# Performance work log

Hardware: AMD Instinct MI355X
Metric: run time of the kernel (lower is better)

Reference implementation:

```python
import jax, jax.numpy as jnp
import numpy as np

B = 512; D = 128; NL = 16; LAYERS = 4; H = 4; HD = D // H
MAX_D = 128; MAX_E = 512
N_DRUG = 25600; N_ENZ = 153600


def setup_inputs() -> dict:
    key = jax.random.key(0)
    ks = jax.random.split(key, 40)
    it = iter(range(40))
    def nrm(shape, scale=0.02):
        return jax.random.normal(ks[next(it)], shape, jnp.float32) * scale
    inp = {}
    inp["drug_k"] = jax.random.normal(ks[next(it)], (N_DRUG, D), jnp.float32)
    inp["drug_v"] = jax.random.normal(ks[next(it)], (N_DRUG, D), jnp.float32)
    inp["enzyme_k"] = jax.random.normal(ks[next(it)], (N_ENZ, D), jnp.float32)
    inp["enzyme_v"] = jax.random.normal(ks[next(it)], (N_ENZ, D), jnp.float32)
    inp["drug_batch"] = jnp.sort(jax.random.randint(ks[next(it)], (N_DRUG,), 0, B))
    inp["enzyme_batch"] = jnp.sort(jax.random.randint(ks[next(it)], (N_ENZ,), 0, B))
    inp["latents"] = nrm((1, NL, D), 1.0)
    inp["wq_d"] = nrm((LAYERS, D, D)); inp["bq_d"] = jnp.zeros((LAYERS, D), jnp.float32)
    inp["wq_e"] = nrm((LAYERS, D, D)); inp["bq_e"] = jnp.zeros((LAYERS, D), jnp.float32)
    inp["mha_d_w"] = nrm((LAYERS, 3 * D, D)); inp["mha_d_b"] = jnp.zeros((LAYERS, 3 * D), jnp.float32)
    inp["mha_d_ow"] = nrm((LAYERS, D, D)); inp["mha_d_ob"] = jnp.zeros((LAYERS, D), jnp.float32)
    inp["mha_e_w"] = nrm((LAYERS, 3 * D, D)); inp["mha_e_b"] = jnp.zeros((LAYERS, 3 * D), jnp.float32)
    inp["mha_e_ow"] = nrm((LAYERS, D, D)); inp["mha_e_ob"] = jnp.zeros((LAYERS, D), jnp.float32)
    inp["ln1_g"] = jnp.ones((LAYERS, D), jnp.float32); inp["ln1_b"] = jnp.zeros((LAYERS, D), jnp.float32)
    inp["ln2_g"] = jnp.ones((LAYERS, D), jnp.float32); inp["ln2_b"] = jnp.zeros((LAYERS, D), jnp.float32)
    inp["ffn_w1"] = nrm((LAYERS, 2 * D, D)); inp["ffn_b1"] = jnp.zeros((LAYERS, 2 * D), jnp.float32)
    inp["ffn_w2"] = nrm((LAYERS, D, 2 * D)); inp["ffn_b2"] = jnp.zeros((LAYERS, D), jnp.float32)
    inp["head_w1"] = nrm((D, D * NL)); inp["head_b1"] = jnp.zeros((D,), jnp.float32)
    inp["head_w2"] = nrm((1, D)); inp["head_b2"] = jnp.zeros((1,), jnp.float32)
    return inp


def to_dense(x, batch, max_len):
    # PyG to_dense_batch: ragged [N, D] -> padded [B, max_len, D] + bool mask
    ones = jnp.ones_like(batch)
    counts = jax.ops.segment_sum(ones, batch, num_segments=B)
    starts = jnp.concatenate([jnp.zeros((1,), counts.dtype), jnp.cumsum(counts)[:-1]])
    pos = jnp.arange(batch.shape[0]) - starts[batch]
    dense = jnp.zeros((B, max_len, x.shape[-1]), x.dtype).at[batch, pos].set(x)
    mask = jnp.zeros((B, max_len), bool).at[batch, pos].set(True)
    return dense, mask


def layer_norm(x, g, b):
    m = x.mean(-1, keepdims=True)
    v = ((x - m) ** 2).mean(-1, keepdims=True)
    return (x - m) / jnp.sqrt(v + 1e-5) * g + b


def mha(q, k, v, mask, w, b, ow, ob):
    # torch nn.MultiheadAttention (batch_first) with key_padding_mask (~mask = ignore)
    wq, wk, wv = w[:D], w[D:2 * D], w[2 * D:]
    bq, bk, bv = b[:D], b[D:2 * D], b[2 * D:]
    qh = (q @ wq.T + bq).reshape(q.shape[0], -1, H, HD)
    kh = (k @ wk.T + bk).reshape(k.shape[0], -1, H, HD)
    vh = (v @ wv.T + bv).reshape(v.shape[0], -1, H, HD)
    s = jnp.einsum('bqhd,bkhd->bhqk', qh, kh) / jnp.sqrt(jnp.float32(HD))
    s = jnp.where(mask[:, None, None, :], s, jnp.float32(-1e9))
    a = jax.nn.softmax(s, axis=-1)
    o = jnp.einsum('bhqk,bkhd->bqhd', a, vh).reshape(q.shape[0], -1, D)
    return o @ ow.T + ob


def forward_impl(drug_k, drug_v, enzyme_k, enzyme_v, latents,
                 wq_d, bq_d, wq_e, bq_e,
                 mha_d_w, mha_d_b, mha_d_ow, mha_d_ob,
                 mha_e_w, mha_e_b, mha_e_ow, mha_e_ob,
                 ln1_g, ln1_b, ln2_g, ln2_b,
                 ffn_w1, ffn_b1, ffn_w2, ffn_b2,
                 head_w1, head_b1, head_w2, head_b2,
                 drug_batch, enzyme_batch):
    dK, dM = to_dense(drug_k, drug_batch, MAX_D)
    dV, _ = to_dense(drug_v, drug_batch, MAX_D)
    eK, eM = to_dense(enzyme_k, enzyme_batch, MAX_E)
    eV, _ = to_dense(enzyme_v, enzyme_batch, MAX_E)
    lat = jnp.broadcast_to(latents, (B, NL, D))
    for l in range(LAYERS):
        nl = layer_norm(lat, ln1_g[l], ln1_b[l])
        q_d = nl @ wq_d[l].T + bq_d[l]
        q_e = nl @ wq_e[l].T + bq_e[l]
        ad = mha(q_d, dK, dV, dM, mha_d_w[l], mha_d_b[l], mha_d_ow[l], mha_d_ob[l])
        ae = mha(q_e, eK, eV, eM, mha_e_w[l], mha_e_b[l], mha_e_ow[l], mha_e_ob[l])
        lat = lat + ad + ae
        h = layer_norm(lat, ln2_g[l], ln2_b[l])
        h = jax.nn.relu(h @ ffn_w1[l].T + ffn_b1[l]) @ ffn_w2[l].T + ffn_b2[l]
        lat = lat + h
    flat = lat.reshape(B, NL * D)
    h = jax.nn.relu(flat @ head_w1.T + head_b1)
    return jax.nn.softplus(h @ head_w2.T + head_b2)[:, 0]


def reference(drug_k, drug_v, enzyme_k, enzyme_v, drug_batch, enzyme_batch, latents,
              wq_d, bq_d, wq_e, bq_e,
              mha_d_w, mha_d_b, mha_d_ow, mha_d_ob,
              mha_e_w, mha_e_b, mha_e_ow, mha_e_ob,
              ln1_g, ln1_b, ln2_g, ln2_b,
              ffn_w1, ffn_b1, ffn_w2, ffn_b2,
              head_w1, head_b1, head_w2, head_b2):
    return forward_impl(drug_k, drug_v, enzyme_k, enzyme_v, latents,
                        wq_d, bq_d, wq_e, bq_e,
                        mha_d_w, mha_d_b, mha_d_ow, mha_d_ob,
                        mha_e_w, mha_e_b, mha_e_ow, mha_e_ob,
                        ln1_g, ln1_b, ln2_g, ln2_b,
                        ffn_w1, ffn_b1, ffn_w2, ffn_b2,
                        head_w1, head_b1, head_w2, head_b2,
                        drug_batch, enzyme_batch)
```

## Files before the change

kernel.cpp:

```cpp
#include <hip/hip_runtime.h>
#include <math.h>

#define NL 16
#define DD 128

typedef __attribute__((ext_vector_type(8))) short short8;
typedef __attribute__((ext_vector_type(4))) float floatx4;

union U8 { short8 v; unsigned short s[8]; };

__device__ __forceinline__ unsigned short f2bf(float x) {
  union { float f; unsigned u; } v; v.f = x; return (unsigned short)(v.u >> 16);
}
__device__ __forceinline__ float bf2f(unsigned short s) {
  union { unsigned u; float f; } v; v.u = ((unsigned)s) << 16; return v.f;
}

__global__ void seg_kernel(const int* __restrict__ db, int nd,
                           const int* __restrict__ eb, int ne,
                           int* __restrict__ seg) {
  const int* arr = (blockIdx.x == 0) ? db : eb;
  int n = (blockIdx.x == 0) ? nd : ne;
  int* start = seg + blockIdx.x * 1024;
  int* cnt = start + 512;
  int b = threadIdx.x;
  if (b < 512) {
    int lo = 0, hi = n;
    while (lo < hi) { int mid = (lo + hi) >> 1; if (arr[mid] < b) lo = mid + 1; else hi = mid; }
    int s = lo;
    lo = s; hi = n;
    while (lo < hi) { int mid = (lo + hi) >> 1; if (arr[mid] < b + 1) lo = mid + 1; else hi = mid; }
    start[b] = s; cnt[b] = lo - s;
  }
}

__global__ void init_lat_kernel(const float* __restrict__ latents, float* __restrict__ lat) {
  int i = blockIdx.x * blockDim.x + threadIdx.x;
  ((float4*)lat)[i] = ((const float4*)latents)[i & 511];
}

__global__ void cvt4_kernel(const float* __restrict__ a, unsigned short* __restrict__ da, int na4,
                            const float* __restrict__ b, unsigned short* __restrict__ db, int nb4,
                            const float* __restrict__ c, unsigned short* __restrict__ dc, int nc4,
                            const float* __restrict__ d, unsigned short* __restrict__ dd, int nd4) {
  int i = blockIdx.x * blockDim.x + threadIdx.x;
  const float* s; unsigned short* o; int r;
  if (i < na4)                        { s = a; o = da; r = i; }
  else if (i < na4 + nb4)             { s = b; o = db; r = i - na4; }
  else if (i < na4 + nb4 + nc4)       { s = c; o = dc; r = i - na4 - nb4; }
  else if (i < na4 + nb4 + nc4 + nd4) { s = d; o = dd; r = i - na4 - nb4 - nc4; }
  else return;
  float4 v = ((const float4*)s)[r];
  ushort4 u = { f2bf(v.x), f2bf(v.y), f2bf(v.z), f2bf(v.w) };
  ((ushort4*)o)[r] = u;
}

__global__ void cvtw_kernel(const float* __restrict__ mw_d, const float* __restrict__ ow_d,
                            const float* __restrict__ mw_e, const float* __restrict__ ow_e,
                            const float* __restrict__ w1, const float* __restrict__ w2,
                            unsigned short* __restrict__ Wbf) {
  int l = blockIdx.x >> 7, blk = blockIdx.x & 127;
  int idx = blk * 1024 + threadIdx.x * 4;
  const float* src; int off;
  if (idx < 16384)      { src = mw_d + (size_t)l * 49152 + 32768; off = idx; }
  else if (idx < 32768) { src = ow_d + (size_t)l * 16384; off = idx - 16384; }
  else if (idx < 49152) { src = mw_e + (size_t)l * 49152 + 32768; off = idx - 32768; }
  else if (idx < 65536) { src = ow_e + (size_t)l * 16384; off = idx - 49152; }
  else if (idx < 98304) { src = w1 + (size_t)l * 32768; off = idx - 65536; }
  else                  { src = w2 + (size_t)l * 32768; off = idx - 98304; }
  float4 v = *(const float4*)(src + off);
  ushort4 o = { f2bf(v.x), f2bf(v.y), f2bf(v.z), f2bf(v.w) };
  *(ushort4*)(Wbf + (size_t)l * 131072 + idx) = o;
}

__global__ __launch_bounds__(256) void fold_kernel(
    const float* __restrict__ wq_d, const float* __restrict__ bq_d,
    const float* __restrict__ wq_e, const float* __restrict__ bq_e,
    const float* __restrict__ mw_d, const float* __restrict__ mb_d,
    const float* __restrict__ mw_e, const float* __restrict__ mb_e,
    float* __restrict__ Wqf, float* __restrict__ bqf) {
  __shared__ __align__(16) float sMW[2048];
  const int pb = blockIdx.x >> 3, rg = blockIdx.x & 7;
  const int l = pb >> 1, p = pb & 1;
  const float* wq = (p == 0 ? wq_d : wq_e) + (size_t)l * 16384;
  const float* bq = (p == 0 ? bq_d : bq_e) + l * 128;
  const float* mw = (p == 0 ? mw_d : mw_e) + (size_t)l * 49152;
  const float* mb = (p == 0 ? mb_d : mb_e) + l * 384;
  const float scale = 0.17677669529663687f;
  const int tid = threadIdx.x;
  {
    const float4* src = (const float4*)(mw + rg * 2048);
    ((float4*)sMW)[tid] = src[tid];
    ((float4*)sMW)[tid + 256] = src[tid + 256];
  }
  __syncthreads();
  const int j = tid & 127, ih = tid >> 7;
  float acc[8];
#pragma unroll
  for (int r = 0; r < 8; ++r) acc[r] = 0.f;
#pragma unroll 4
  for (int k = 0; k < 128; ++k) {
    float wv = wq[k * 128 + j];
#pragma unroll
    for (int r = 0; r < 8; ++r) acc[r] += sMW[(ih * 8 + r) * 128 + k] * wv;
  }
  float* W = Wqf + (size_t)pb * 16384 + (rg * 16 + ih * 8) * 128 + j;
#pragma unroll
  for (int r = 0; r < 8; ++r) W[r * 128] = acc[r] * scale;
  if (rg == 0 && tid < 128) {
    float s = 0.f;
    const float* mr = mw + tid * 128;
    for (int k = 0; k < 128; ++k) s += mr[k] * bq[k];
    bqf[pb * 128 + tid] = (s + mb[tid]) * scale;
  }
}

__global__ __launch_bounds__(256) void wt_kernel(
    const float* __restrict__ Wqf, const float* __restrict__ bqf,
    const float* __restrict__ mw_d, const float* __restrict__ mw_e,
    unsigned short* __restrict__ WtB, float* __restrict__ bt) {
  const int l = blockIdx.x >> 3, p = (blockIdx.x >> 2) & 1, h = blockIdx.x & 3;
  const float* wqf = Wqf + (size_t)(l * 2 + p) * 16384 + (h * 32) * 128;
  const float* wk  = (p == 0 ? mw_d : mw_e) + (size_t)l * 49152 + 16384 + (h * 32) * 128;
  const float* bqv = bqf + (l * 2 + p) * 128 + h * 32;
  __shared__ __align__(16) float sWq[4096];
  __shared__ __align__(16) float sWk[4096];
  __shared__ float sBq[32];
  const int tid = threadIdx.x;
  for (int i = tid; i < 1024; i += 256) {
    ((float4*)sWq)[i] = ((const float4*)wqf)[i];
    ((float4*)sWk)[i] = ((const float4*)wk)[i];
  }
  if (tid < 32) sBq[tid] = bqv[tid];
  __syncthreads();
  const int d = tid & 127, kh = tid >> 7;
  const int n = p * 512 + h * 128 + d;
  const int tn = n >> 4, m = n & 15;
  unsigned short* outl = WtB + (size_t)l * 131072;
#pragma unroll
  for (int kc = 0; kc < 4; ++kc) {
    int k0 = kh * 64 + kc * 16;
    float acc[16];
#pragma unroll
    for (int kk = 0; kk < 16; ++kk) acc[kk] = 0.f;
    for (int j = 0; j < 32; ++j) {
      float wkd = sWk[j * 128 + d];
#pragma unroll
      for (int kk = 0; kk < 16; ++kk) acc[kk] += sWq[j * 128 + k0 + kk] * wkd;
    }
#pragma unroll
    for (int kk = 0; kk < 16; ++kk) {
      int k = k0 + kk;
      int c = k >> 5, quad = (k >> 3) & 3, j8 = k & 7;
      int lane = quad * 16 + m;
      outl[(((size_t)tn * 4 + c) * 64 + lane) * 8 + j8] = f2bf(acc[kk]);
    }
  }
  if (kh == 0) {
    float a = 0.f;
    for (int j = 0; j < 32; ++j) a += sBq[j] * sWk[j * 128 + d];
    bt[l * 1024 + n] = a;
  }
}

__global__ __launch_bounds__(256) void qtilde_kernel(
    const float* __restrict__ lat,
    const float* __restrict__ lng, const float* __restrict__ lnb,
    const unsigned short* __restrict__ WtBl, const float* __restrict__ btl,
    unsigned short* __restrict__ Qt) {
  __shared__ __align__(16) unsigned short sNL[16 * 136];
  const int tid = threadIdx.x;
  const int b = blockIdx.x;
  {
    int q = tid >> 4, li = tid & 15, d0 = li * 8;
    const float* xr = lat + ((size_t)b * NL + q) * DD + d0;
    float x[8];
    *(float4*)(x) = *(const float4*)(xr);
    *(float4*)(x + 4) = *(const float4*)(xr + 4);
    float s1 = 0.f, s2 = 0.f;
#pragma unroll
    for (int j = 0; j < 8; ++j) { s1 += x[j]; s2 += x[j] * x[j]; }
#pragma unroll
    for (int o = 1; o < 16; o <<= 1) { s1 += __shfl_xor(s1, o); s2 += __shfl_xor(s2, o); }
    float mean = s1 * (1.f / 128.f);
    float var = s2 * (1.f / 128.f) - mean * mean;
    float rstd = rsqrtf(var + 1e-5f);
    float y[8];
#pragma unroll
    for (int j = 0; j < 8; ++j)
      y[j] = (x[j] - mean) * rstd * lng[d0 + j] + lnb[d0 + j];
    ushort4 o0 = { f2bf(y[0]), f2bf(y[1]), f2bf(y[2]), f2bf(y[3]) };
    ushort4 o1 = { f2bf(y[4]), f2bf(y[5]), f2bf(y[6]), f2bf(y[7]) };
    *(ushort4*)(sNL + q * 136 + d0) = o0;
    *(ushort4*)(sNL + q * 136 + d0 + 4) = o1;
  }
  __syncthreads();
  const int lane = tid & 63, w = tid >> 6, m = lane & 15, quad = lane >> 4;
  short8 aF[4];
  {
    const unsigned short* arow = sNL + m * 136 + quad * 8;
#pragma unroll
    for (int c = 0; c < 4; ++c) aF[c] = *(const short8*)(arow + c * 32);
  }
  unsigned short* qtb = Qt + (size_t)b * 16384;
#pragma unroll
  for (int t = 0; t < 16; ++t) {
    int tn = w * 16 + t;
    floatx4 acc = (floatx4){0.f, 0.f, 0.f, 0.f};
#pragma unroll
    for (int c = 0; c < 4; ++c) {
      short8 bF = *(const short8*)(WtBl + (((size_t)tn * 4 + c) * 64 + lane) * 8);
      acc = __builtin_amdgcn_mfma_f32_16x16x32_bf16(aF[c], bF, acc, 0, 0, 0);
    }
    int n = tn * 16 + m;
    float bb = btl[n];
    int p = n >> 9, h = (n >> 7) & 3, d = n & 127;
    unsigned short* op = qtb + (p * 64 + h * 16) * 128 + d;
#pragma unroll
    for (int r = 0; r < 4; ++r) op[(quad * 4 + r) * 128] = f2bf(acc[r] + bb);
  }
}

__global__ __launch_bounds__(256, 4) void attn3_kernel(
    const unsigned short* __restrict__ Kd, const unsigned short* __restrict__ Vd,
    const unsigned short* __restrict__ Ke, const unsigned short* __restrict__ Ve,
    const int* __restrict__ seg,
    const unsigned short* __restrict__ Qt,
    unsigned short* __restrict__ part_d, float* __restrict__ l_d,
    unsigned short* __restrict__ part_e, float* __restrict__ l_e) {
  __shared__ __align__(16) unsigned short sK[32 * 136];
  __shared__ __align__(16) unsigned short sV[128 * 40];
  __shared__ __align__(16) unsigned short sP[64 * 40];
  const int tid = threadIdx.x;
  const int bi = blockIdx.x;

  const unsigned short* Kp; const unsigned short* Vp;
  const unsigned short* qt;
  unsigned short* part; float* lpart;
  int len, st;
  if (bi < 2048) {
    int b = bi >> 2, sp = bi & 3;
    int n = seg[1536 + b]; if (n > 512) n = 512;
    int chunk = (n + 3) >> 2;
    int begin = sp * chunk;
    len = n - begin; if (len > chunk) len = chunk; if (len < 0) len = 0;
    st = seg[1024 + b] + begin;
    Kp = Ke; Vp = Ve;
    qt = Qt + ((size_t)b * 2 + 1) * 8192;
    part = part_e + (size_t)bi * 8192;
    lpart = l_e + (size_t)bi * 64;
  } else {
    int b = bi - 2048;
    int n = seg[512 + b]; if (n > 128) n = 128;
    len = n;
    st = seg[b];
    Kp = Kd; Vp = Vd;
    qt = Qt + (size_t)b * 2 * 8192;
    part = part_d + (size_t)b * 8192;
    lpart = l_d + (size_t)b * 64;
  }

  const int lane = tid & 63;
  const int w = tid >> 6;
  const int m = lane & 15;
  const int quad = lane >> 4;

  short8 qA[4];
  {
    const unsigned short* qrow = qt + (size_t)(w * 16 + m) * 128 + quad * 8;
#pragma unroll
    for (int c = 0; c < 4; ++c) qA[c] = *(const short8*)(qrow + c * 32);
  }

  floatx4 oA[8];
#pragma unroll
  for (int i = 0; i < 8; ++i) oA[i] = (floatx4){0.f, 0.f, 0.f, 0.f};
  float lp[4] = {0.f, 0.f, 0.f, 0.f};

  short8 rK[2], rV[2];
  const short8 z8 = {0, 0, 0, 0, 0, 0, 0, 0};
  auto load_tile = [&](int t0) {
    int nv = len - t0; if (nv > 32) nv = 32;
#pragma unroll
    for (int it = 0; it < 2; ++it) {
      int f = tid + it * 256;
      int tok = f >> 4, d8 = f & 15;
      rK[it] = (tok < nv) ? *(const short8*)(Kp + (size_t)(st + t0 + tok) * 128 + d8 * 8) : z8;
    }
#pragma unroll
    for (int it = 0; it < 2; ++it) {
      int f = tid + it * 256;
      int tok = f & 31, d8 = f >> 5;
      rV[it] = (tok < nv) ? *(const short8*)(Vp + (size_t)(st + t0 + tok) * 128 + d8 * 8) : z8;
    }
  };
  auto store_tile = [&]() {
#pragma unroll
    for (int it = 0; it < 2; ++it) {
      int f = tid + it * 256;
      int tok = f >> 4, d8 = f & 15;
      *(short8*)(sK + tok * 136 + d8 * 8) = rK[it];
    }
#pragma unroll
    for (int it = 0; it < 2; ++it) {
      int f = tid + it * 256;
      int tok = f & 31, d8 = f >> 5;
      U8 u; u.v = rV[it];
#pragma unroll
      for (int j = 0; j < 8; ++j) sV[(d8 * 8 + j) * 40 + tok] = u.s[j];
    }
  };

  if (len > 0) load_tile(0);
  for (int t0 = 0; t0 < len; t0 += 32) {
    __syncthreads();
    store_tile();
    __syncthreads();
    if (t0 + 32 < len) load_tile(t0 + 32);
    int nv = len - t0; if (nv > 32) nv = 32;
    floatx4 sS[2];
    sS[0] = (floatx4){0.f, 0.f, 0.f, 0.f};
    sS[1] = (floatx4){0.f, 0.f, 0.f, 0.f};
#pragma unroll
    for (int g = 0; g < 2; ++g)
#pragma unroll
      for (int c = 0; c < 4; ++c) {
        short8 kB = *(const short8*)(sK + (g * 16 + m) * 136 + c * 32 + quad * 8);
        sS[g] = __builtin_amdgcn_mfma_f32_16x16x32_bf16(qA[c], kB, sS[g], 0, 0, 0);
      }
#pragma unroll
    for (int g = 0; g < 2; ++g) {
      bool valid = (g * 16 + m) < nv;
#pragma unroll
      for (int r = 0; r < 4; ++r) {
        float p = valid ? __expf(sS[g][r]) : 0.f;
        lp[r] += p;
        sP[(w * 16 + quad * 4 + r) * 40 + g * 16 + m] = f2bf(p);
      }
    }
    short8 pA = *(const short8*)(sP + (w * 16 + m) * 40 + quad * 8);
#pragma unroll
    for (int dg = 0; dg < 8; ++dg) {
      short8 vB = *(const short8*)(sV + (dg * 16 + m) * 40 + quad * 8);
      oA[dg] = __builtin_amdgcn_mfma_f32_16x16x32_bf16(pA, vB, oA[dg], 0, 0, 0);
    }
  }

#pragma unroll
  for (int r = 0; r < 4; ++r) {
    float v = lp[r];
    v += __shfl_xor(v, 1); v += __shfl_xor(v, 2);
    v += __shfl_xor(v, 4); v += __shfl_xor(v, 8);
    lp[r] = v;
  }
  if (m == 0) {
#pragma unroll
    for (int r = 0; r < 4; ++r)
      lpart[w * 16 + quad * 4 + r] = lp[r];
  }
#pragma unroll
  for (int dg = 0; dg < 8; ++dg)
#pragma unroll
    for (int r = 0; r < 4; ++r)
      part[(w * 16 + quad * 4 + r) * 128 + dg * 16 + m] = f2bf(oA[dg][r]);
}

__global__ __launch_bounds__(256) void post_kernel(
    const unsigned short* __restrict__ pd, const float* __restrict__ ldv,
    const unsigned short* __restrict__ pe, const float* __restrict__ lev,
    const unsigned short* __restrict__ Wl,
    const float* __restrict__ bv_d, const float* __restrict__ ob_d,
    const float* __restrict__ bv_e, const float* __restrict__ ob_e,
    const float* __restrict__ ln2g, const float* __restrict__ ln2b,
    const float* __restrict__ b1, const float* __restrict__ b2,
    float* __restrict__ lat) {
  const unsigned short* wv_d = Wl;
  const unsigned short* ow_d = Wl + 16384;
  const unsigned short* wv_e = Wl + 32768;
  const unsigned short* ow_e = Wl + 49152;
  const unsigned short* w1   = Wl + 65536;
  const unsigned short* w2   = Wl + 98304;

  __shared__ __align__(16) unsigned short sX[64 * 136];
  __shared__ __align__(16) unsigned short sVH[16 * 136];
  __shared__ __align__(16) unsigned short sF[16 * 264];
  __shared__ __align__(16) float sAcc[16 * 132];
  __shared__ float sLd[64], sLe[64];

  const int tid = threadIdx.x;
  const int b = blockIdx.x;
  const int lane = tid & 63;
  const int w = tid >> 6;
  const int m = lane & 15;
  const int quad = lane >> 4;

  if (tid < 64) {
    float v = ldv[(size_t)b * 64 + tid];
    sLd[tid] = (v > 0.f) ? 1.f / v : 0.f;
  } else if (tid < 128) {
    int r = tid - 64;
    float v = lev[((size_t)b * 4 + 0) * 64 + r] + lev[((size_t)b * 4 + 1) * 64 + r]
            + lev[((size_t)b * 4 + 2) * 64 + r] + lev[((size_t)b * 4 + 3) * 64 + r];
    sLe[r] = (v > 0.f) ? 1.f / v : 0.f;
  }
  __syncthreads();
  {
    const ushort4* src = (const ushort4*)(pd + (size_t)b * 8192);
#pragma unroll
    for (int it = 0; it < 8; ++it) {
      int f = tid + it * 256;
      int row = f >> 5, d = (f & 31) * 4;
      ushort4 u = src[f];
      float sc = sLd[row];
      ushort4 o = { f2bf(bf2f(u.x) * sc), f2bf(bf2f(u.y) * sc),
                    f2bf(bf2f(u.z) * sc), f2bf(bf2f(u.w) * sc) };
      *(ushort4*)(sX + row * 136 + d) = o;
    }
  }
  __syncthreads();
  {
    short8 aF[4];
    const unsigned short* arow = sX + (w * 16 + m) * 136 + quad * 8;
#pragma unroll
    for (int c = 0; c < 4; ++c) aF[c] = *(const short8*)(arow + c * 32);
#pragma unroll
    for (int t = 0; t < 2; ++t) {
      int n = w * 32 + t * 16 + m;
      floatx4 acc = (floatx4){0.f, 0.f, 0.f, 0.f};
      const unsigned short* brow = wv_d + n * 128 + quad * 8;
#pragma unroll
      for (int c = 0; c < 4; ++c)
        acc = __builtin_amdgcn_mfma_f32_16x16x32_bf16(aF[c], *(const short8*)(brow + c * 32), acc, 0, 0, 0);
      float bb = bv_d[n];
#pragma unroll
      for (int r = 0; r < 4; ++r) sVH[(quad * 4 + r) * 136 + n] = f2bf(acc[r] + bb);
    }
  }
  __syncthreads();
  {
    short8 aF[4];
    const unsigned short* arow = sVH + m * 136 + quad * 8;
#pragma unroll
    for (int c = 0; c < 4; ++c) aF[c] = *(const short8*)(arow + c * 32);
#pragma unroll
    for (int t = 0; t < 2; ++t) {
      int n = w * 32 + t * 16 + m;
      floatx4 acc = (floatx4){0.f, 0.f, 0.f, 0.f};
      const unsigned short* brow = ow_d + n * 128 + quad * 8;
#pragma unroll
      for (int c = 0; c < 4; ++c)
        acc = __builtin_amdgcn_mfma_f32_16x16x32_bf16(aF[c], *(const short8*)(brow + c * 32), acc, 0, 0, 0);
      float bb = ob_d[n];
#pragma unroll
      for (int r = 0; r < 4; ++r) {
        int q = quad * 4 + r;
        sAcc[q * 132 + n] = lat[(size_t)b * 2048 + q * 128 + n] + acc[r] + bb;
      }
    }
  }
  __syncthreads();
  {
    const ushort4* s0 = (const ushort4*)(pe + ((size_t)b * 4 + 0) * 8192);
    const ushort4* s1 = (const ushort4*)(pe + ((size_t)b * 4 + 1) * 8192);
    const ushort4* s2 = (const ushort4*)(pe + ((size_t)b * 4 + 2) * 8192);
    const ushort4* s3 = (const ushort4*)(pe + ((size_t)b * 4 + 3) * 8192);
#pragma unroll
    for (int it = 0; it < 8; ++it) {
      int f = tid + it * 256;
      int row = f >> 5, d = (f & 31) * 4;
      ushort4 u0 = s0[f], u1 = s1[f], u2 = s2[f], u3 = s3[f];
      float sc = sLe[row];
      ushort4 o = { f2bf((bf2f(u0.x) + bf2f(u1.x) + bf2f(u2.x) + bf2f(u3.x)) * sc),
                    f2bf((bf2f(u0.y) + bf2f(u1.y) + bf2f(u2.y) + bf2f(u3.y)) * sc),
                    f2bf((bf2f(u0.z) + bf2f(u1.z) + bf2f(u2.z) + bf2f(u3.z)) * sc),
                    f2bf((bf2f(u0.w) + bf2f(u1.w) + bf2f(u2.w) + bf2f(u3.w)) * sc) };
      *(ushort4*)(sX + row * 136 + d) = o;
    }
  }
  __syncthreads();
  {
    short8 aF[4];
    const unsigned short* arow = sX + (w * 16 + m) * 136 + quad * 8;
#pragma unroll
    for (int c = 0; c < 4; ++c) aF[c] = *(const short8*)(arow + c * 32);
#pragma unroll
    for (int t = 0; t < 2; ++t) {
      int n = w * 32 + t * 16 + m;
      floatx4 acc = (floatx4){0.f, 0.f, 0.f, 0.f};
      const unsigned short* brow = wv_e + n * 128 + quad * 8;
#pragma unroll
      for (int c = 0; c < 4; ++c)
        acc = __builtin_amdgcn_mfma_f32_16x16x32_bf16(aF[c], *(const short8*)(brow + c * 32), acc, 0, 0, 0);
      float bb = bv_e[n];
#pragma unroll
      for (int r = 0; r < 4; ++r) sVH[(quad * 4 + r) * 136 + n] = f2bf(acc[r] + bb);
    }
  }
  __syncthreads();
  {
    short8 aF[4];
    const unsigned short* arow = sVH + m * 136 + quad * 8;
#pragma unroll
    for (int c = 0; c < 4; ++c) aF[c] = *(const short8*)(arow + c * 32);
#pragma unroll
    for (int t = 0; t < 2; ++t) {
      int n = w * 32 + t * 16 + m;
      floatx4 acc = (floatx4){0.f, 0.f, 0.f, 0.f};
      const unsigned short* brow = ow_e + n * 128 + quad * 8;
#pragma unroll
      for (int c = 0; c < 4; ++c)
        acc = __builtin_amdgcn_mfma_f32_16x16x32_bf16(aF[c], *(const short8*)(brow + c * 32), acc, 0, 0, 0);
      float bb = ob_e[n];
#pragma unroll
      for (int r = 0; r < 4; ++r) {
        int q = quad * 4 + r;
        sAcc[q * 132 + n] += acc[r] + bb;
      }
    }
  }
  __syncthreads();
  {
    int q = tid >> 4, li = tid & 15, d0 = li * 8;
    float x[8];
#pragma unroll
    for (int j = 0; j < 8; ++j) x[j] = sAcc[q * 132 + d0 + j];
    float s1 = 0.f, s2 = 0.f;
#pragma unroll
    for (int j = 0; j < 8; ++j) { s1 += x[j]; s2 += x[j] * x[j]; }
#pragma unroll
    for (int o = 1; o < 16; o <<= 1) { s1 += __shfl_xor(s1, o); s2 += __shfl_xor(s2, o); }
    float mean = s1 * (1.f / 128.f);
    float var = s2 * (1.f / 128.f) - mean * mean;
    float rstd = rsqrtf(var + 1e-5f);
    float y[8];
#pragma unroll
    for (int j = 0; j < 8; ++j)
      y[j] = (x[j] - mean) * rstd * ln2g[d0 + j] + ln2b[d0 + j];
    ushort4 o0 = { f2bf(y[0]), f2bf(y[1]), f2bf(y[2]), f2bf(y[3]) };
    ushort4 o1 = { f2bf(y[4]), f2bf(y[5]), f2bf(y[6]), f2bf(y[7]) };
    *(ushort4*)(sX + q * 136 + d0) = o0;
    *(ushort4*)(sX + q * 136 + d0 + 4) = o1;
  }
  __syncthreads();
  {
    short8 aF[4];
    const unsigned short* arow = sX + m * 136 + quad * 8;
#pragma unroll
    for (int c = 0; c < 4; ++c) aF[c] = *(const short8*)(arow + c * 32);
#pragma unroll
    for (int t = 0; t < 4; ++t) {
      int n = w * 64 + t * 16 + m;
      floatx4 acc = (floatx4){0.f, 0.f, 0.f, 0.f};
      const unsigned short* brow = w1 + n * 128 + quad * 8;
#pragma unroll
      for (int c = 0; c < 4; ++c)
        acc = __builtin_amdgcn_mfma_f32_16x16x32_bf16(aF[c], *(const short8*)(brow + c * 32), acc, 0, 0, 0);
      float bb = b1[n];
#pragma unroll
      for (int r = 0; r < 4; ++r)
        sF[(quad * 4 + r) * 264 + n] = f2bf(fmaxf(acc[r] + bb, 0.f));
    }
  }
  __syncthreads();
  {
    short8 aF[8];
    const unsigned short* arow = sF + m * 264 + quad * 8;
#pragma unroll
    for (int c = 0; c < 8; ++c) aF[c] = *(const short8*)(arow + c * 32);
#pragma unroll
    for (int t = 0; t < 2; ++t) {
      int n = w * 32 + t * 16 + m;
      floatx4 acc = (floatx4){0.f, 0.f, 0.f, 0.f};
      const unsigned short* brow = w2 + n * 256 + quad * 8;
#pragma unroll
      for (int c = 0; c < 8; ++c)
        acc = __builtin_amdgcn_mfma_f32_16x16x32_bf16(aF[c], *(const short8*)(brow + c * 32), acc, 0, 0, 0);
      float bb = b2[n];
#pragma unroll
      for (int r = 0; r < 4; ++r) {
        int q = quad * 4 + r;
        lat[(size_t)b * 2048 + q * 128 + n] = sAcc[q * 132 + n] + acc[r] + bb;
      }
    }
  }
}

__global__ __launch_bounds__(256) void head_kernel(const float* __restrict__ lat,
                                                   const float* __restrict__ w1,
                                                   const float* __restrict__ b1,
                                                   const float* __restrict__ w2,
                                                   const float* __restrict__ b2,
                                                   float* __restrict__ out) {
  __shared__ __align__(16) float sX[2048];
  __shared__ float sH[128];
  const int tid = threadIdx.x;
  const int b = blockIdx.x;
  {
    const float4* src = (const float4*)(lat + (size_t)b * 2048);
#pragma unroll
    for (int it = 0; it < 2; ++it) ((float4*)sX)[tid + it * 256] = src[tid + it * 256];
  }
  __syncthreads();
  {
    int o = tid >> 1, kh = tid & 1;
    float a = 0.f;
    const float* wr = w1 + (size_t)o * 2048 + kh * 1024;
    const float* xb = sX + kh * 1024;
    for (int k4 = 0; k4 < 256; ++k4) {
      float4 w4 = *(const float4*)(wr + k4 * 4);
      float4 x4 = *(const float4*)(xb + k4 * 4);
      a += w4.x * x4.x + w4.y * x4.y + w4.z * x4.z + w4.w * x4.w;
    }
    a += __shfl_xor(a, 1);
    if (kh == 0) sH[o] = fmaxf(a + b1[o], 0.f);
  }
  __syncthreads();
  if (tid < 64) {
    float a = sH[tid] * w2[tid] + sH[tid + 64] * w2[tid + 64];
#pragma unroll
    for (int o = 1; o < 64; o <<= 1) a += __shfl_xor(a, o);
    if (tid == 0) {
      float x = a + b2[0];
      out[b] = (x > 20.f) ? x : log1pf(__expf(x));
    }
  }
}

extern "C" void kernel_launch(void* const* d_in, const int* in_sizes, int n_in,
                              void* d_out, int out_size, void* d_ws, size_t ws_size,
                              hipStream_t stream) {
  const float* drug_k  = (const float*)d_in[0];
  const float* drug_v  = (const float*)d_in[1];
  const float* enz_k   = (const float*)d_in[2];
  const float* enz_v   = (const float*)d_in[3];
  const int*   drug_b  = (const int*)d_in[4];
  const int*   enz_b   = (const int*)d_in[5];
  const float* latents = (const float*)d_in[6];
  const float* wq_d    = (const float*)d_in[7];
  const float* bq_d    = (const float*)d_in[8];
  const float* wq_e    = (const float*)d_in[9];
  const float* bq_e    = (const float*)d_in[10];
  const float* mha_d_w = (const float*)d_in[11];
  const float* mha_d_b = (const float*)d_in[12];
  const float* mha_d_ow= (const float*)d_in[13];
  const float* mha_d_ob= (const float*)d_in[14];
  const float* mha_e_w = (const float*)d_in[15];
  const float* mha_e_b = (const float*)d_in[16];
  const float* mha_e_ow= (const float*)d_in[17];
  const float* mha_e_ob= (const float*)d_in[18];
  const float* ln1_g   = (const float*)d_in[19];
  const float* ln1_b   = (const float*)d_in[20];
  const float* ln2_g   = (const float*)d_in[21];
  const float* ln2_b   = (const float*)d_in[22];
  const float* ffn_w1  = (const float*)d_in[23];
  const float* ffn_b1  = (const float*)d_in[24];
  const float* ffn_w2  = (const float*)d_in[25];
  const float* ffn_b2  = (const float*)d_in[26];
  const float* head_w1 = (const float*)d_in[27];
  const float* head_b1 = (const float*)d_in[28];
  const float* head_w2 = (const float*)d_in[29];
  const float* head_b2 = (const float*)d_in[30];
  float* out = (float*)d_out;

  const int n_dk = in_sizes[0];
  const int n_ek = in_sizes[2];

  int* seg = (int*)d_ws;
  float* fws = (float*)d_ws;
  float* Wqf = fws + 2048;
  float* bqf = Wqf + 131072;
  float* lat = bqf + 1024;
  float* l_d = lat + 1048576;
  float* l_e = l_d + 32768;
  unsigned short* Qt     = (unsigned short*)(l_e + 131072);
  unsigned short* part_d = Qt + 8388608;
  unsigned short* part_e = part_d + 4194304;
  unsigned short* Kd_bf  = part_e + 16777216;
  unsigned short* Vd_bf  = Kd_bf + n_dk;
  unsigned short* Ke_bf  = Vd_bf + n_dk;
  unsigned short* Ve_bf  = Ke_bf + n_ek;
  unsigned short* Wbf    = Ve_bf + n_ek;
  unsigned short* WtB    = Wbf + 524288;
  float* bt              = (float*)(WtB + 524288);

  seg_kernel<<<2, 512, 0, stream>>>(drug_b, in_sizes[4], enz_b, in_sizes[5], seg);
  init_lat_kernel<<<1024, 256, 0, stream>>>(latents, lat);
  fold_kernel<<<64, 256, 0, stream>>>(wq_d, bq_d, wq_e, bq_e,
                                      mha_d_w, mha_d_b, mha_e_w, mha_e_b, Wqf, bqf);
  wt_kernel<<<32, 256, 0, stream>>>(Wqf, bqf, mha_d_w, mha_e_w, WtB, bt);
  {
    int na4 = n_dk / 4, nc4 = n_ek / 4;
    int tot = na4 * 2 + nc4 * 2;
    cvt4_kernel<<<(tot + 255) / 256, 256, 0, stream>>>(
        drug_k, Kd_bf, na4, drug_v, Vd_bf, na4, enz_k, Ke_bf, nc4, enz_v, Ve_bf, nc4);
  }
  cvtw_kernel<<<512, 256, 0, stream>>>(mha_d_w, mha_d_ow, mha_e_w, mha_e_ow,
                                       ffn_w1, ffn_w2, Wbf);
  for (int l = 0; l < 4; ++l) {
    qtilde_kernel<<<512, 256, 0, stream>>>(lat, ln1_g + l * 128, ln1_b + l * 128,
        WtB + (size_t)l * 131072, bt + l * 1024, Qt);
    attn3_kernel<<<2560, 256, 0, stream>>>(Kd_bf, Vd_bf, Ke_bf, Ve_bf, seg,
        Qt, part_d, l_d, part_e, l_e);
    post_kernel<<<512, 256, 0, stream>>>(part_d, l_d, part_e, l_e,
        Wbf + (size_t)l * 131072,
        mha_d_b + l * 384 + 256, mha_d_ob + l * 128,
        mha_e_b + l * 384 + 256, mha_e_ob + l * 128,
        ln2_g + l * 128, ln2_b + l * 128,
        ffn_b1 + l * 256, ffn_b2 + l * 128,
        lat);
  }
  head_kernel<<<512, 256, 0, stream>>>(lat, head_w1, head_b1, head_w2, head_b2, out);
}
```

Measured before the change: 623.2 us.

## Fuse K/V bf16 conversion into first attention pass, fuse qtilde into post, MFMA head

Removes the standalone K/V fp32-to-bf16 conversion kernel. The first attention layer now reads fp32 K/V, converts it in registers and writes bf16 copies for later layers to reuse. Layer 0 uses a single qtilde launch with a shared Q (stride 0), since all batches start from identical latents. Later layers compute the next LayerNorm and Q projection at the end of post_kernel, which removes per-layer launches and a re-read of lat. The head is rewritten as a bf16 MFMA GEMM over 16-row tiles, with a rotated sV store order to reduce LDS bank conflicts; the trade-off is extra branching and lower precision in the head.

```diff
diff --git a/kernel.cpp b/kernel.cpp
--- a/kernel.cpp
+++ b/kernel.cpp
@@ -37,22 +37,6 @@
 __global__ void init_lat_kernel(const float* __restrict__ latents, float* __restrict__ lat) {
   int i = blockIdx.x * blockDim.x + threadIdx.x;
   ((float4*)lat)[i] = ((const float4*)latents)[i & 511];
-}
-
-__global__ void cvt4_kernel(const float* __restrict__ a, unsigned short* __restrict__ da, int na4,
-                            const float* __restrict__ b, unsigned short* __restrict__ db, int nb4,
-                            const float* __restrict__ c, unsigned short* __restrict__ dc, int nc4,
-                            const float* __restrict__ d, unsigned short* __restrict__ dd, int nd4) {
-  int i = blockIdx.x * blockDim.x + threadIdx.x;
-  const float* s; unsigned short* o; int r;
-  if (i < na4)                        { s = a; o = da; r = i; }
-  else if (i < na4 + nb4)             { s = b; o = db; r = i - na4; }
-  else if (i < na4 + nb4 + nc4)       { s = c; o = dc; r = i - na4 - nb4; }
-  else if (i < na4 + nb4 + nc4 + nd4) { s = d; o = dd; r = i - na4 - nb4 - nc4; }
-  else return;
-  float4 v = ((const float4*)s)[r];
-  ushort4 u = { f2bf(v.x), f2bf(v.y), f2bf(v.z), f2bf(v.w) };
-  ((ushort4*)o)[r] = u;
 }
 
 __global__ void cvtw_kernel(const float* __restrict__ mw_d, const float* __restrict__ ow_d,
@@ -73,6 +57,13 @@
   *(ushort4*)(Wbf + (size_t)l * 131072 + idx) = o;
 }
 
+__global__ void cvth_kernel(const float* __restrict__ w1, unsigned short* __restrict__ dst) {
+  int i = blockIdx.x * blockDim.x + threadIdx.x;
+  float4 v = ((const float4*)w1)[i];
+  ushort4 o = { f2bf(v.x), f2bf(v.y), f2bf(v.z), f2bf(v.w) };
+  ((ushort4*)dst)[i] = o;
+}
+
 __global__ __launch_bounds__(256) void fold_kernel(
     const float* __restrict__ wq_d, const float* __restrict__ bq_d,
     const float* __restrict__ wq_e, const float* __restrict__ bq_e,
@@ -222,10 +213,12 @@
 }
 
 __global__ __launch_bounds__(256, 4) void attn3_kernel(
-    const unsigned short* __restrict__ Kd, const unsigned short* __restrict__ Vd,
-    const unsigned short* __restrict__ Ke, const unsigned short* __restrict__ Ve,
+    const float* __restrict__ Kd32, const float* __restrict__ Vd32,
+    const float* __restrict__ Ke32, const float* __restrict__ Ve32,
+    unsigned short* __restrict__ Kd, unsigned short* __restrict__ Vd,
+    unsigned short* __restrict__ Ke, unsigned short* __restrict__ Ve,
     const int* __restrict__ seg,
-    const unsigned short* __restrict__ Qt,
+    const unsigned short* __restrict__ Qt, int qstride, int cvt,
     unsigned short* __restrict__ part_d, float* __restrict__ l_d,
     unsigned short* __restrict__ part_e, float* __restrict__ l_e) {
   __shared__ __align__(16) unsigned short sK[32 * 136];
@@ -234,7 +227,8 @@
   const int tid = threadIdx.x;
   const int bi = blockIdx.x;
 
-  const unsigned short* Kp; const unsigned short* Vp;
+  const float* Kp32; const float* Vp32;
+  unsigned short* KpB; unsigned short* VpB;
   const unsigned short* qt;
   unsigned short* part; float* lpart;
   int len, st;
@@ -245,8 +239,8 @@
     int begin = sp * chunk;
     len = n - begin; if (len > chunk) len = chunk; if (len < 0) len = 0;
     st = seg[1024 + b] + begin;
-    Kp = Ke; Vp = Ve;
-    qt = Qt + ((size_t)b * 2 + 1) * 8192;
+    Kp32 = Ke32; Vp32 = Ve32; KpB = Ke; VpB = Ve;
+    qt = Qt + (size_t)b * qstride + 8192;
     part = part_e + (size_t)bi * 8192;
     lpart = l_e + (size_t)bi * 64;
   } else {
@@ -254,8 +248,8 @@
     int n = seg[512 + b]; if (n > 128) n = 128;
     len = n;
     st = seg[b];
-    Kp = Kd; Vp = Vd;
-    qt = Qt + (size_t)b * 2 * 8192;
+    Kp32 = Kd32; Vp32 = Vd32; KpB = Kd; VpB = Vd;
+    qt = Qt + (size_t)b * qstride;
     part = part_d + (size_t)b * 8192;
     lpart = l_d + (size_t)b * 64;
   }
@@ -281,17 +275,46 @@
   const short8 z8 = {0, 0, 0, 0, 0, 0, 0, 0};
   auto load_tile = [&](int t0) {
     int nv = len - t0; if (nv > 32) nv = 32;
-#pragma unroll
-    for (int it = 0; it < 2; ++it) {
-      int f = tid + it * 256;
-      int tok = f >> 4, d8 = f & 15;
-      rK[it] = (tok < nv) ? *(const short8*)(Kp + (size_t)(st + t0 + tok) * 128 + d8 * 8) : z8;
-    }
-#pragma unroll
-    for (int it = 0; it < 2; ++it) {
-      int f = tid + it * 256;
-      int tok = f & 31, d8 = f >> 5;
-      rV[it] = (tok < nv) ? *(const short8*)(Vp + (size_t)(st + t0 + tok) * 128 + d8 * 8) : z8;
+    if (cvt) {
+#pragma unroll
+      for (int it = 0; it < 2; ++it) {
+        int f = tid + it * 256;
+        int tok = f >> 4, d8 = f & 15;
+        if (tok < nv) {
+          size_t g = (size_t)(st + t0 + tok) * 128 + d8 * 8;
+          const float* s = Kp32 + g;
+          float4 a = *(const float4*)s, c = *(const float4*)(s + 4);
+          U8 u;
+          u.s[0]=f2bf(a.x); u.s[1]=f2bf(a.y); u.s[2]=f2bf(a.z); u.s[3]=f2bf(a.w);
+          u.s[4]=f2bf(c.x); u.s[5]=f2bf(c.y); u.s[6]=f2bf(c.z); u.s[7]=f2bf(c.w);
+          rK[it] = u.v;
+          *(short8*)(KpB + g) = u.v;
+        } else rK[it] = z8;
+      }
+#pragma unroll
+      for (int it = 0; it < 2; ++it) {
+        int f = tid + it * 256;
+        int tok = f >> 4, d8 = f & 15;
+        if (tok < nv) {
+          size_t g = (size_t)(st + t0 + tok) * 128 + d8 * 8;
+          const float* s = Vp32 + g;
+          float4 a = *(const float4*)s, c = *(const float4*)(s + 4);
+          U8 u;
+          u.s[0]=f2bf(a.x); u.s[1]=f2bf(a.y); u.s[2]=f2bf(a.z); u.s[3]=f2bf(a.w);
+          u.s[4]=f2bf(c.x); u.s[5]=f2bf(c.y); u.s[6]=f2bf(c.z); u.s[7]=f2bf(c.w);
+          rV[it] = u.v;
+          *(short8*)(VpB + g) = u.v;
+        } else rV[it] = z8;
+      }
+    } else {
+#pragma unroll
+      for (int it = 0; it < 2; ++it) {
+        int f = tid + it * 256;
+        int tok = f >> 4, d8 = f & 15;
+        size_t g = (size_t)(st + t0 + tok) * 128 + d8 * 8;
+        rK[it] = (tok < nv) ? *(const short8*)(KpB + g) : z8;
+        rV[it] = (tok < nv) ? *(const short8*)(VpB + g) : z8;
+      }
     }
   };
   auto store_tile = [&]() {
@@ -300,14 +323,12 @@
       int f = tid + it * 256;
       int tok = f >> 4, d8 = f & 15;
       *(short8*)(sK + tok * 136 + d8 * 8) = rK[it];
-    }
-#pragma unroll
-    for (int it = 0; it < 2; ++it) {
-      int f = tid + it * 256;
-      int tok = f & 31, d8 = f >> 5;
       U8 u; u.v = rV[it];
 #pragma unroll
-      for (int j = 0; j < 8; ++j) sV[(d8 * 8 + j) * 40 + tok] = u.s[j];
+      for (int i = 0; i < 8; ++i) {
+        int j = (i + d8) & 7;
+        sV[(d8 * 8 + j) * 40 + tok] = u.s[j];
+      }
     }
   };
 
@@ -373,7 +394,10 @@
     const float* __restrict__ bv_e, const float* __restrict__ ob_e,
     const float* __restrict__ ln2g, const float* __restrict__ ln2b,
     const float* __restrict__ b1, const float* __restrict__ b2,
-    float* __restrict__ lat) {
+    float* __restrict__ lat,
+    const float* __restrict__ lng1, const float* __restrict__ lnb1,
+    const unsigned short* __restrict__ WtB_next, const float* __restrict__ bt_next,
+    unsigned short* __restrict__ Qt) {
   const unsigned short* wv_d = Wl;
   const unsigned short* ow_d = Wl + 16384;
   const unsigned short* wv_e = Wl + 32768;
@@ -579,50 +603,111 @@
 #pragma unroll
       for (int r = 0; r < 4; ++r) {
         int q = quad * 4 + r;
-        lat[(size_t)b * 2048 + q * 128 + n] = sAcc[q * 132 + n] + acc[r] + bb;
-      }
-    }
-  }
-}
-
-__global__ __launch_bounds__(256) void head_kernel(const float* __restrict__ lat,
-                                                   const float* __restrict__ w1,
-                                                   const float* __restrict__ b1,
-                                                   const float* __restrict__ w2,
-                                                   const float* __restrict__ b2,
-                                                   float* __restrict__ out) {
-  __shared__ __align__(16) float sX[2048];
-  __shared__ float sH[128];
+        float fin = sAcc[q * 132 + n] + acc[r] + bb;
+        lat[(size_t)b * 2048 + q * 128 + n] = fin;
+        sAcc[q * 132 + n] = fin;
+      }
+    }
+  }
+  if (WtB_next) {
+    __syncthreads();
+    {
+      int q = tid >> 4, li = tid & 15, d0 = li * 8;
+      float x[8];
+#pragma unroll
+      for (int j = 0; j < 8; ++j) x[j] = sAcc[q * 132 + d0 + j];
+      float s1 = 0.f, s2 = 0.f;
+#pragma unroll
+      for (int j = 0; j < 8; ++j) { s1 += x[j]; s2 += x[j] * x[j]; }
+#pragma unroll
+      for (int o = 1; o < 16; o <<= 1) { s1 += __shfl_xor(s1, o); s2 += __shfl_xor(s2, o); }
+      float mean = s1 * (1.f / 128.f);
+      float var = s2 * (1.f / 128.f) - mean * mean;
+      float rstd = rsqrtf(var + 1e-5f);
+      float y[8];
+#pragma unroll
+      for (int j = 0; j < 8; ++j)
+        y[j] = (x[j] - mean) * rstd * lng1[d0 + j] + lnb1[d0 + j];
+      ushort4 o0 = { f2bf(y[0]), f2bf(y[1]), f2bf(y[2]), f2bf(y[3]) };
+      ushort4 o1 = { f2bf(y[4]), f2bf(y[5]), f2bf(y[6]), f2bf(y[7]) };
+      *(ushort4*)(sX + q * 136 + d0) = o0;
+      *(ushort4*)(sX + q * 136 + d0 + 4) = o1;
+    }
+    __syncthreads();
+    short8 aF[4];
+    const unsigned short* arow = sX + m * 136 + quad * 8;
+#pragma unroll
+    for (int c = 0; c < 4; ++c) aF[c] = *(const short8*)(arow + c * 32);
+    unsigned short* qtb = Qt + (size_t)b * 16384;
+#pragma unroll
+    for (int t = 0; t < 16; ++t) {
+      int tn = w * 16 + t;
+      floatx4 acc = (floatx4){0.f, 0.f, 0.f, 0.f};
+#pragma unroll
+      for (int c = 0; c < 4; ++c) {
+        short8 bF = *(const short8*)(WtB_next + (((size_t)tn * 4 + c) * 64 + lane) * 8);
+        acc = __builtin_amdgcn_mfma_f32_16x16x32_bf16(aF[c], bF, acc, 0, 0, 0);
+      }
+      int n = tn * 16 + m;
+      float bb = bt_next[n];
+      int p = n >> 9, h = (n >> 7) & 3, d = n & 127;
+      unsigned short* op = qtb + (p * 64 + h * 16) * 128 + d;
+#pragma unroll
+      for (int r = 0; r < 4; ++r) op[(quad * 4 + r) * 128] = f2bf(acc[r] + bb);
+    }
+  }
+}
+
+__global__ __launch_bounds__(256) void head_kernel(
+    const float* __restrict__ lat, const unsigned short* __restrict__ w1b,
+    const float* __restrict__ b1, const float* __restrict__ w2,
+    const float* __restrict__ b2, float* __restrict__ out) {
+  __shared__ __align__(16) unsigned short sA[16 * 2056];
+  __shared__ float sW[4][16];
   const int tid = threadIdx.x;
-  const int b = blockIdx.x;
-  {
-    const float4* src = (const float4*)(lat + (size_t)b * 2048);
-#pragma unroll
-    for (int it = 0; it < 2; ++it) ((float4*)sX)[tid + it * 256] = src[tid + it * 256];
-  }
-  __syncthreads();
-  {
-    int o = tid >> 1, kh = tid & 1;
-    float a = 0.f;
-    const float* wr = w1 + (size_t)o * 2048 + kh * 1024;
-    const float* xb = sX + kh * 1024;
-    for (int k4 = 0; k4 < 256; ++k4) {
-      float4 w4 = *(const float4*)(wr + k4 * 4);
-      float4 x4 = *(const float4*)(xb + k4 * 4);
-      a += w4.x * x4.x + w4.y * x4.y + w4.z * x4.z + w4.w * x4.w;
-    }
-    a += __shfl_xor(a, 1);
-    if (kh == 0) sH[o] = fmaxf(a + b1[o], 0.f);
-  }
-  __syncthreads();
-  if (tid < 64) {
-    float a = sH[tid] * w2[tid] + sH[tid + 64] * w2[tid + 64];
-#pragma unroll
-    for (int o = 1; o < 64; o <<= 1) a += __shfl_xor(a, o);
-    if (tid == 0) {
-      float x = a + b2[0];
-      out[b] = (x > 20.f) ? x : log1pf(__expf(x));
-    }
+  const int b0 = blockIdx.x * 16;
+  for (int i = tid; i < 8192; i += 256) {
+    int bb = i >> 9, c4 = i & 511;
+    float4 v = ((const float4*)(lat + (size_t)(b0 + bb) * 2048))[c4];
+    ushort4 u = { f2bf(v.x), f2bf(v.y), f2bf(v.z), f2bf(v.w) };
+    *(ushort4*)(sA + bb * 2056 + c4 * 4) = u;
+  }
+  __syncthreads();
+  const int lane = tid & 63, w = tid >> 6, m = lane & 15, quad = lane >> 4;
+  float s[4] = {0.f, 0.f, 0.f, 0.f};
+#pragma unroll
+  for (int t = 0; t < 2; ++t) {
+    int nt = w * 2 + t;
+    int o = nt * 16 + m;
+    floatx4 acc = (floatx4){0.f, 0.f, 0.f, 0.f};
+    const unsigned short* brow = w1b + (size_t)o * 2048 + quad * 8;
+    const unsigned short* arow = sA + m * 2056 + quad * 8;
+    for (int c = 0; c < 64; ++c) {
+      short8 aF = *(const short8*)(arow + c * 32);
+      short8 bF = *(const short8*)(brow + c * 32);
+      acc = __builtin_amdgcn_mfma_f32_16x16x32_bf16(aF, bF, acc, 0, 0, 0);
+    }
+    float w2v = w2[o];
+    float b1v = b1[o];
+#pragma unroll
+    for (int r = 0; r < 4; ++r)
+      s[r] += fmaxf(acc[r] + b1v, 0.f) * w2v;
+  }
+#pragma unroll
+  for (int r = 0; r < 4; ++r) {
+    float v = s[r];
+    v += __shfl_xor(v, 1); v += __shfl_xor(v, 2);
+    v += __shfl_xor(v, 4); v += __shfl_xor(v, 8);
+    s[r] = v;
+  }
+  if (m == 0) {
+#pragma unroll
+    for (int r = 0; r < 4; ++r) sW[w][quad * 4 + r] = s[r];
+  }
+  __syncthreads();
+  if (tid < 16) {
+    float x = sW[0][tid] + sW[1][tid] + sW[2][tid] + sW[3][tid] + b2[0];
+    out[b0 + tid] = (x > 20.f) ? x : log1pf(__expf(x));
   }
 }
 
@@ -682,32 +767,33 @@
   unsigned short* Wbf    = Ve_bf + n_ek;
   unsigned short* WtB    = Wbf + 524288;
   float* bt              = (float*)(WtB + 524288);
+  unsigned short* w1h    = (unsigned short*)(bt + 4096);
 
   seg_kernel<<<2, 512, 0, stream>>>(drug_b, in_sizes[4], enz_b, in_sizes[5], seg);
   init_lat_kernel<<<1024, 256, 0, stream>>>(latents, lat);
   fold_kernel<<<64, 256, 0, stream>>>(wq_d, bq_d, wq_e, bq_e,
                                       mha_d_w, mha_d_b, mha_e_w, mha_e_b, Wqf, bqf);
   wt_kernel<<<32, 256, 0, stream>>>(Wqf, bqf, mha_d_w, mha_e_w, WtB, bt);
-  {
-    int na4 = n_dk / 4, nc4 = n_ek / 4;
-    int tot = na4 * 2 + nc4 * 2;
-    cvt4_kernel<<<(tot + 255) / 256, 256, 0, stream>>>(
-        drug_k, Kd_bf, na4, drug_v, Vd_bf, na4, enz_k, Ke_bf, nc4, enz_v, Ve_bf, nc4);
-  }
   cvtw_kernel<<<512, 256, 0, stream>>>(mha_d_w, mha_d_ow, mha_e_w, mha_e_ow,
                                        ffn_w1, ffn_w2, Wbf);
+  cvth_kernel<<<256, 256, 0, stream>>>(head_w1, w1h);
+  qtilde_kernel<<<1, 256, 0, stream>>>(lat, ln1_g, ln1_b, WtB, bt, Qt);
   for (int l = 0; l < 4; ++l) {
-    qtilde_kernel<<<512, 256, 0, stream>>>(lat, ln1_g + l * 128, ln1_b + l * 128,
-        WtB + (size_t)l * 131072, bt + l * 1024, Qt);
-    attn3_kernel<<<2560, 256, 0, stream>>>(Kd_bf, Vd_bf, Ke_bf, Ve_bf, seg,
-        Qt, part_d, l_d, part_e, l_e);
+    attn3_kernel<<<2560, 256, 0, stream>>>(drug_k, drug_v, enz_k, enz_v,
+        Kd_bf, Vd_bf, Ke_bf, Ve_bf, seg,
+        Qt, (l == 0) ? 0 : 16384, (l == 0) ? 1 : 0,
+        part_d, l_d, part_e, l_e);
+    const unsigned short* wtn = (l < 3) ? (WtB + (size_t)(l + 1) * 131072) : nullptr;
+    const float* btn = (l < 3) ? (bt + (l + 1) * 1024) : nullptr;
     post_kernel<<<512, 256, 0, stream>>>(part_d, l_d, part_e, l_e,
         Wbf + (size_t)l * 131072,
         mha_d_b + l * 384 + 256, mha_d_ob + l * 128,
         mha_e_b + l * 384 + 256, mha_e_ob + l * 128,
         ln2_g + l * 128, ln2_b + l * 128,
         ffn_b1 + l * 256, ffn_b2 + l * 128,
-        lat);
-  }
-  head_kernel<<<512, 256, 0, stream>>>(lat, head_w1, head_b1, head_w2, head_b2, out);
-}
+        lat,
+        ln1_g + (l + 1 < 4 ? (l + 1) * 128 : 0), ln1_b + (l + 1 < 4 ? (l + 1) * 128 : 0),
+        wtn, btn, Qt);
+  }
+  head_kernel<<<32, 256, 0, stream>>>(lat, w1h, head_b1, head_w2, head_b2, out);
+}
```

After: 645.6 us. +3.6%, slower.
